# Optimization experiments

Measured on AMD Instinct MI355X. Metric: run time of the kernel, lower is better.

## Reference

```python
import jax, jax.numpy as jnp
import numpy as np


def monarch_linear(x, w1, w2, bias, out_features):
    """Monarch structured linear: permute + block-diag + permute + block-diag.
    x: (B, n_in); w1: (k, q, p); w2: (l, s, r) with k*q == l*r.
    """
    b, n = x.shape
    k, q, p = w1.shape
    l, s, r = w2.shape
    n_ext = k * p
    if n_ext > n:  # preprocess: zero-pad input to in_features_extended
        x = jnp.pad(x, ((0, 0), (0, n_ext - n)))
    # first block-diagonal matmul: (B,k,p) x (k,q,p) -> (B,k,q)
    out1 = jnp.einsum('bkp,kqp->bkq', x.reshape(b, k, p), w1)
    # permutation: view (B, k*q) as (B, r, l) then transpose -> (B, l, r)
    out1 = out1.reshape(b, r, l).transpose(0, 2, 1)
    # second block-diagonal matmul: (B,l,r) x (l,s,r) -> (B,l,s)
    out2 = jnp.einsum('blr,lsr->bls', out1, w2)
    # final permutation: (B,l,s) -> (B,s,l) -> (B, s*l), then slice to out_features
    out = out2.transpose(0, 2, 1).reshape(b, s * l)[:, :out_features]
    return out + bias


def setup_inputs() -> dict:
    key = jax.random.key(0)
    ks = jax.random.split(key, 14)
    B = 65536
    specs = {
        'x': (B, 1, 28, 28),
        'fc1_w1': (15, 27, 53), 'fc1_w2': (15, 27, 27), 'fc1_b': (392,),
        'fc2_w1': (15, 9, 27), 'fc2_w2': (15, 9, 9), 'fc2_b': (128,),
        'fc3_w1': (15, 5, 9), 'fc3_w2': (15, 5, 5), 'fc3_b': (64,),
        'fc4_w1': (15, 1, 5), 'fc4_w2': (15, 1, 1), 'fc4_b': (10,),
    }
    out = {}
    for i, (name, shape) in enumerate(specs.items()):
        v = jax.random.normal(ks[i], shape, dtype=jnp.float32)
        if name != 'x':
            v = v * 0.1  # keep activations in a sane range through 4 layers
        out[name] = v
    return out


def reference(x, fc1_w1, fc1_w2, fc1_b, fc2_w1, fc2_w2, fc2_b,
              fc3_w1, fc3_w2, fc3_b, fc4_w1, fc4_w2, fc4_b):
    gelu = lambda t: jax.nn.gelu(t, approximate=False)  # torch F.gelu default = exact erf
    h = x.reshape(x.shape[0], -1)  # flatten (B,1,28,28) -> (B,784)
    h = gelu(monarch_linear(h, fc1_w1, fc1_w2, fc1_b, 392))
    h = gelu(monarch_linear(h, fc2_w1, fc2_w2, fc2_b, 128))
    h = gelu(monarch_linear(h, fc3_w1, fc3_w2, fc3_b, 64))
    h = monarch_linear(h, fc4_w1, fc4_w2, fc4_b, 10)
    return jax.nn.log_softmax(h, axis=1)
```

## Files before the change

kernel.cpp:

```cpp
#include <hip/hip_runtime.h>
#include <hip/hip_bf16.h>

typedef unsigned short u16;
typedef unsigned int   u32;

__device__ __forceinline__ float b2f(u16 v){ return __uint_as_float(((u32)v) << 16); }
__device__ __forceinline__ u16   f2b(float f){
  u32 u = __float_as_uint(f);
  u += 0x7fffu + ((u >> 16) & 1u);
  return (u16)(u >> 16);
}
__device__ __forceinline__ float gelu_exact(float x){
  return 0.5f * x * (1.0f + erff(x * 0.70710678118654752440f));
}

__global__ __launch_bounds__(256) void k_prep_w1(
    const float* __restrict__ w1, float* __restrict__ wtg)
{
  int tid = blockIdx.x*256 + threadIdx.x;
  for (int e = tid; e < 15*54*28; e += gridDim.x*256){
    int kk = e / 1512, rem = e - kk*1512;
    int p = rem / 28, j = rem - p*28;
    wtg[e] = (p < 53 && j < 27) ? w1[(kk*27 + j)*53 + p] : 0.0f;
  }
}

__global__ __launch_bounds__(256, 5) void k_fc1a(
    const float* __restrict__ x, const float* __restrict__ wtg,
    u16* __restrict__ act, int base, int Bc)
{
  __shared__ u32 xsu[256*27];
  const int tid = threadIdx.x;
  const int k   = blockIdx.y;
  const int rowloc = blockIdx.x * 256;

  #pragma unroll 4
  for (int i = 0; i < 27; ++i){
    int e = i*256 + tid;
    int r = e / 27, c2 = e - r*27;
    int col = k*53 + 2*c2;
    const size_t rowoff = (size_t)(base + rowloc + r)*784;
    float v0 = 0.f, v1 = 0.f;
    if (col < 784) v0 = x[rowoff + col];
    if (2*c2+1 < 53 && col+1 < 784) v1 = x[rowoff + col + 1];
    xsu[e] = (u32)f2b(v0) | ((u32)f2b(v1) << 16);
  }
  __syncthreads();

  float acc[28];
  #pragma unroll
  for (int j = 0; j < 28; ++j) acc[j] = 0.0f;

  const float* __restrict__ wk = wtg + (size_t)k*1512;
  const u32* xrow = &xsu[tid*27];
  #pragma unroll
  for (int pp = 0; pp < 27; ++pp){
    const u32 xv2 = xrow[pp];
    const float x0 = __uint_as_float(xv2 << 16);
    const float x1 = __uint_as_float(xv2 & 0xffff0000u);
    const float4* wa = (const float4*)(wk + 56*pp);
    const float4* wb = (const float4*)(wk + 56*pp + 28);
    #pragma unroll
    for (int i = 0; i < 7; ++i){
      const float4 a = wa[i];
      const float4 b = wb[i];
      acc[4*i+0] = fmaf(a.x, x0, fmaf(b.x, x1, acc[4*i+0]));
      acc[4*i+1] = fmaf(a.y, x0, fmaf(b.y, x1, acc[4*i+1]));
      acc[4*i+2] = fmaf(a.z, x0, fmaf(b.z, x1, acc[4*i+2]));
      acc[4*i+3] = fmaf(a.w, x0, fmaf(b.w, x1, acc[4*i+3]));
    }
  }
  const int r0 = rowloc + tid;
  #pragma unroll
  for (int j = 0; j < 27; ++j)
    act[(size_t)(k*27 + j)*Bc + r0] = f2b(acc[j]);
}

__global__ __launch_bounds__(256) void k_fc1b(
    const float* __restrict__ w2, const float* __restrict__ b1,
    u16* act, int Bc)
{
  __shared__ __align__(16) float w2s[27*28];
  __shared__ float b1s[27];
  const int tid = threadIdx.x;
  const int l   = blockIdx.y;
  for (int e = tid; e < 27*28; e += 256){
    int s = e / 28, r = e - s*28;
    w2s[e] = (r < 27) ? w2[(l*27 + s)*27 + r] : 0.0f;
  }
  if (tid < 27){
    int m = tid*15 + l;
    b1s[tid] = (m < 392) ? b1[m] : 0.0f;
  }
  __syncthreads();

  const int row = blockIdx.x*256 + tid;
  float t[28];
  #pragma unroll
  for (int r = 0; r < 27; ++r) t[r] = b2f(act[(size_t)(r*15 + l)*Bc + row]);
  t[27] = 0.0f;
  #pragma unroll
  for (int s = 0; s < 27; ++s){
    const float* wp = &w2s[s*28];
    float va = 0.f, vb = 0.f;
    #pragma unroll
    for (int i = 0; i < 7; ++i){
      const float4 w = *(const float4*)&wp[4*i];
      va = fmaf(w.x, t[4*i+0], va); vb = fmaf(w.y, t[4*i+1], vb);
      va = fmaf(w.z, t[4*i+2], va); vb = fmaf(w.w, t[4*i+3], vb);
    }
    const int m = s*15 + l;
    float h = (m < 392) ? gelu_exact(va + vb + b1s[s]) : 0.0f;
    act[(size_t)m*Bc + row] = f2b(h);
  }
}

__global__ __launch_bounds__(256) void k_fc2a(
    const u16* __restrict__ h1t, const float* __restrict__ w1_2,
    u16* __restrict__ o2t, int Bc)
{
  __shared__ __align__(16) float ws[9*28];
  const int tid = threadIdx.x;
  const int k   = blockIdx.y;
  for (int e = tid; e < 9*28; e += 256){
    int j = e / 28, p = e - j*28;
    ws[e] = (p < 27) ? w1_2[(k*9 + j)*27 + p] : 0.0f;
  }
  __syncthreads();

  const int row = blockIdx.x*256 + tid;
  float hb[28];
  #pragma unroll
  for (int p = 0; p < 27; ++p) hb[p] = b2f(h1t[(size_t)(k*27 + p)*Bc + row]);
  hb[27] = 0.0f;
  #pragma unroll
  for (int j = 0; j < 9; ++j){
    const float* wp = &ws[j*28];
    float va = 0.f, vb = 0.f;
    #pragma unroll
    for (int i = 0; i < 7; ++i){
      const float4 w = *(const float4*)&wp[4*i];
      va = fmaf(w.x, hb[4*i+0], va); vb = fmaf(w.y, hb[4*i+1], vb);
      va = fmaf(w.z, hb[4*i+2], va); vb = fmaf(w.w, hb[4*i+3], vb);
    }
    o2t[(size_t)(k*9 + j)*Bc + row] = f2b(va + vb);
  }
}

__global__ __launch_bounds__(256) void k_fc2b(
    const u16* __restrict__ o2t, const float* __restrict__ w2_2,
    const float* __restrict__ b2, u16* __restrict__ h2t, int Bc)
{
  __shared__ float ws[9*9];
  __shared__ float b2s[9];
  const int tid = threadIdx.x;
  const int l   = blockIdx.y;
  if (tid < 81) ws[tid] = w2_2[l*81 + tid];
  if (tid < 9){
    int m = tid*15 + l;
    b2s[tid] = (m < 128) ? b2[m] : 0.0f;
  }
  __syncthreads();

  const int row = blockIdx.x*256 + tid;
  float t[9];
  #pragma unroll
  for (int r = 0; r < 9; ++r) t[r] = b2f(o2t[(size_t)(r*15 + l)*Bc + row]);
  #pragma unroll
  for (int s = 0; s < 9; ++s){
    const float* wp = &ws[s*9];
    float v = 0.f;
    #pragma unroll
    for (int r = 0; r < 9; ++r) v = fmaf(wp[r], t[r], v);
    const int m = s*15 + l;
    float h = (m < 128) ? gelu_exact(v + b2s[s]) : 0.0f;
    h2t[(size_t)m*Bc + row] = f2b(h);
  }
}

__global__ __launch_bounds__(256) void k_fc3a(
    const u16* __restrict__ h2t, const float* __restrict__ w1_3,
    u16* __restrict__ o3t, int Bc)
{
  __shared__ float ws[5*9];
  const int tid = threadIdx.x;
  const int k   = blockIdx.y;
  if (tid < 45) ws[tid] = w1_3[k*45 + tid];
  __syncthreads();

  const int row = blockIdx.x*256 + tid;
  float hb[9];
  #pragma unroll
  for (int p = 0; p < 9; ++p) hb[p] = b2f(h2t[(size_t)(k*9 + p)*Bc + row]);
  #pragma unroll
  for (int j = 0; j < 5; ++j){
    const float* wp = &ws[j*9];
    float v = 0.f;
    #pragma unroll
    for (int p = 0; p < 9; ++p) v = fmaf(wp[p], hb[p], v);
    o3t[(size_t)(k*5 + j)*Bc + row] = f2b(v);
  }
}

__global__ __launch_bounds__(256) void k_fc3b4(
    const u16* __restrict__ o3t,
    const float* __restrict__ w2_3, const float* __restrict__ b3,
    const float* __restrict__ w1_4, const float* __restrict__ w2_4, const float* __restrict__ b4,
    float* __restrict__ out, int base, int Bc)
{
  __shared__ __align__(16) float w23s[75*8];
  __shared__ float b3s[64];
  __shared__ float w14s[10*8];
  __shared__ float w24s[10];
  __shared__ float b4s[10];
  __shared__ float outS[256*10];
  const int tid = threadIdx.x;
  for (int e = tid; e < 75*8; e += 256){ int a=e/8, r=e-a*8; w23s[e] = (r<5)? w2_3[a*5+r] : 0.f; }
  for (int e = tid; e < 64;   e += 256) b3s[e] = b3[e];
  for (int e = tid; e < 80;   e += 256){ int c=e/8, p=e-c*8; w14s[e] = (p<5)? w1_4[c*5+p] : 0.f; }
  if (tid < 10){ w24s[tid] = w2_4[tid]; b4s[tid] = b4[tid]; }
  __syncthreads();

  const int rloc = blockIdx.x*256 + tid;

  float sacc[10];
  #pragma unroll
  for (int c = 0; c < 10; ++c) sacc[c] = 0.0f;

  #pragma unroll
  for (int l = 0; l < 15; ++l){
    float t[5];
    #pragma unroll
    for (int r = 0; r < 5; ++r) t[r] = b2f(o3t[(size_t)(r*15 + l)*Bc + rloc]);
    #pragma unroll
    for (int s = 0; s < 5; ++s){
      const int m = s*15 + l;
      if (m < 50){
        const float* wp = &w23s[(l*5 + s)*8];
        float v = 0.f;
        v = fmaf(wp[0], t[0], v); v = fmaf(wp[1], t[1], v);
        v = fmaf(wp[2], t[2], v); v = fmaf(wp[3], t[3], v);
        v = fmaf(wp[4], t[4], v);
        const float h = gelu_exact(v + b3s[m]);
        const int c = m / 5, p = m - (m/5)*5;
        sacc[c] = fmaf(h, w14s[c*8 + p], sacc[c]);
      }
    }
  }
  float v[10];
  #pragma unroll
  for (int c = 0; c < 10; ++c) v[c] = fmaf(sacc[c], w24s[c], b4s[c]);

  float mx = v[0];
  #pragma unroll
  for (int c = 1; c < 10; ++c) mx = fmaxf(mx, v[c]);
  float sum = 0.f;
  #pragma unroll
  for (int c = 0; c < 10; ++c) sum += expf(v[c] - mx);
  const float lse = mx + logf(sum);
  #pragma unroll
  for (int c = 0; c < 10; ++c) outS[tid*10 + c] = v[c] - lse;
  __syncthreads();
  const size_t blockOut = (size_t)(base + blockIdx.x*256) * 10;
  #pragma unroll
  for (int i = 0; i < 10; ++i){
    int e = i*256 + tid;
    out[blockOut + e] = outS[e];
  }
}

extern "C" void kernel_launch(void* const* d_in, const int* in_sizes, int n_in,
                              void* d_out, int out_size, void* d_ws, size_t ws_size,
                              hipStream_t stream)
{
  const float* x     = (const float*)d_in[0];
  const float* f1w1  = (const float*)d_in[1];
  const float* f1w2  = (const float*)d_in[2];
  const float* f1b   = (const float*)d_in[3];
  const float* f2w1  = (const float*)d_in[4];
  const float* f2w2  = (const float*)d_in[5];
  const float* f2b   = (const float*)d_in[6];
  const float* f3w1  = (const float*)d_in[7];
  const float* f3w2  = (const float*)d_in[8];
  const float* f3b   = (const float*)d_in[9];
  const float* f4w1  = (const float*)d_in[10];
  const float* f4w2  = (const float*)d_in[11];
  const float* f4b   = (const float*)d_in[12];
  const int B = in_sizes[0] / 784;
  (void)n_in; (void)out_size;

  const size_t wtgBytes = 90880;
  float* wtg = (float*)d_ws;
  u16*  wsAct = (u16*)((char*)d_ws + wtgBytes);

  k_prep_w1<<<dim3(32), 256, 0, stream>>>(f1w1, wtg);

  const size_t perRow = 750 * sizeof(u16);
  int Rc = B;
  if (ws_size - wtgBytes < (size_t)B * perRow){
    size_t rows = (ws_size - wtgBytes) / perRow;
    Rc = (int)(rows & ~(size_t)511);
    if (Rc < 512) Rc = 512;
  }
  for (int base = 0; base < B; base += Rc){
    const int Bc = (B - base < Rc) ? (B - base) : Rc;
    u16* act = wsAct;
    u16* o2t = act + (size_t)405 * Bc;
    u16* h2t = o2t + (size_t)135 * Bc;
    u16* o3t = h2t + (size_t)135 * Bc;
    k_fc1a<<<dim3(Bc/256, 15), 256, 0, stream>>>(x, wtg, act, base, Bc);
    k_fc1b<<<dim3(Bc/256, 15), 256, 0, stream>>>(f1w2, f1b, act, Bc);
    k_fc2a<<<dim3(Bc/256, 15), 256, 0, stream>>>(act, f2w1, o2t, Bc);
    k_fc2b<<<dim3(Bc/256, 15), 256, 0, stream>>>(o2t, f2w2, f2b, h2t, Bc);
    k_fc3a<<<dim3(Bc/256, 15), 256, 0, stream>>>(h2t, f3w1, o3t, Bc);
    k_fc3b4<<<dim3(Bc/256), 256, 0, stream>>>(o3t, f3w2, f3b,
                                              f4w1, f4w2, f4b, (float*)d_out, base, Bc);
  }
}
```

Before: 457.0 us.

## Compute two rows per thread in fc1/fc2a and read weights from global

The fc1a, fc1b and fc2a kernels now launch 128 threads per block, and each thread computes two batch rows. This reuses every weight load across both rows and halves the number of weight fetches per output. The fc1b and fc2a weights are pre-padded once in an extended prep kernel and read directly from global/scalar memory instead of being staged in LDS. The later kernels also drop their LDS weight staging and __syncthreads in favour of direct global reads. The trade-off is higher register pressure, roughly doubled accumulators, and fewer threads per block, which may lower occupancy.

```diff
diff --git a/kernel.cpp b/kernel.cpp
--- a/kernel.cpp
+++ b/kernel.cpp
@@ -14,18 +14,34 @@
   return 0.5f * x * (1.0f + erff(x * 0.70710678118654752440f));
 }
 
-__global__ __launch_bounds__(256) void k_prep_w1(
-    const float* __restrict__ w1, float* __restrict__ wtg)
+#define WTG_OFF   0
+#define W2G_OFF   22720
+#define W12G_OFF  34112
+#define PREP_F    37952
+
+__global__ __launch_bounds__(256) void k_prep(
+    const float* __restrict__ w1, const float* __restrict__ w2,
+    const float* __restrict__ w1_2, float* __restrict__ ws)
 {
   int tid = blockIdx.x*256 + threadIdx.x;
   for (int e = tid; e < 15*54*28; e += gridDim.x*256){
     int kk = e / 1512, rem = e - kk*1512;
     int p = rem / 28, j = rem - p*28;
-    wtg[e] = (p < 53 && j < 27) ? w1[(kk*27 + j)*53 + p] : 0.0f;
-  }
-}
-
-__global__ __launch_bounds__(256, 5) void k_fc1a(
+    ws[WTG_OFF + e] = (p < 53 && j < 27) ? w1[(kk*27 + j)*53 + p] : 0.0f;
+  }
+  for (int e = tid; e < 15*27*28; e += gridDim.x*256){
+    int l = e / 756, rem = e - l*756;
+    int s = rem / 28, r = rem - s*28;
+    ws[W2G_OFF + e] = (r < 27) ? w2[(l*27 + s)*27 + r] : 0.0f;
+  }
+  for (int e = tid; e < 15*9*28; e += gridDim.x*256){
+    int kk = e / 252, rem = e - kk*252;
+    int j = rem / 28, p = rem - j*28;
+    ws[W12G_OFF + e] = (p < 27) ? w1_2[(kk*9 + j)*27 + p] : 0.0f;
+  }
+}
+
+__global__ __launch_bounds__(128, 3) void k_fc1a(
     const float* __restrict__ x, const float* __restrict__ wtg,
     u16* __restrict__ act, int base, int Bc)
 {
@@ -35,8 +51,8 @@
   const int rowloc = blockIdx.x * 256;
 
   #pragma unroll 4
-  for (int i = 0; i < 27; ++i){
-    int e = i*256 + tid;
+  for (int i = 0; i < 54; ++i){
+    int e = i*128 + tid;
     int r = e / 27, c2 = e - r*27;
     int col = k*53 + 2*c2;
     const size_t rowoff = (size_t)(base + rowloc + r)*784;
@@ -47,103 +63,114 @@
   }
   __syncthreads();
 
-  float acc[28];
-  #pragma unroll
-  for (int j = 0; j < 28; ++j) acc[j] = 0.0f;
+  float acc0[28], acc1[28];
+  #pragma unroll
+  for (int j = 0; j < 28; ++j){ acc0[j] = 0.0f; acc1[j] = 0.0f; }
 
   const float* __restrict__ wk = wtg + (size_t)k*1512;
-  const u32* xrow = &xsu[tid*27];
+  const u32* xrow0 = &xsu[tid*27];
+  const u32* xrow1 = &xsu[(tid+128)*27];
   #pragma unroll
   for (int pp = 0; pp < 27; ++pp){
-    const u32 xv2 = xrow[pp];
-    const float x0 = __uint_as_float(xv2 << 16);
-    const float x1 = __uint_as_float(xv2 & 0xffff0000u);
+    const u32 xa = xrow0[pp];
+    const u32 xb = xrow1[pp];
+    const float x00 = __uint_as_float(xa << 16);
+    const float x01 = __uint_as_float(xa & 0xffff0000u);
+    const float x10 = __uint_as_float(xb << 16);
+    const float x11 = __uint_as_float(xb & 0xffff0000u);
     const float4* wa = (const float4*)(wk + 56*pp);
     const float4* wb = (const float4*)(wk + 56*pp + 28);
     #pragma unroll
     for (int i = 0; i < 7; ++i){
       const float4 a = wa[i];
       const float4 b = wb[i];
-      acc[4*i+0] = fmaf(a.x, x0, fmaf(b.x, x1, acc[4*i+0]));
-      acc[4*i+1] = fmaf(a.y, x0, fmaf(b.y, x1, acc[4*i+1]));
-      acc[4*i+2] = fmaf(a.z, x0, fmaf(b.z, x1, acc[4*i+2]));
-      acc[4*i+3] = fmaf(a.w, x0, fmaf(b.w, x1, acc[4*i+3]));
+      acc0[4*i+0] = fmaf(a.x, x00, fmaf(b.x, x01, acc0[4*i+0]));
+      acc0[4*i+1] = fmaf(a.y, x00, fmaf(b.y, x01, acc0[4*i+1]));
+      acc0[4*i+2] = fmaf(a.z, x00, fmaf(b.z, x01, acc0[4*i+2]));
+      acc0[4*i+3] = fmaf(a.w, x00, fmaf(b.w, x01, acc0[4*i+3]));
+      acc1[4*i+0] = fmaf(a.x, x10, fmaf(b.x, x11, acc1[4*i+0]));
+      acc1[4*i+1] = fmaf(a.y, x10, fmaf(b.y, x11, acc1[4*i+1]));
+      acc1[4*i+2] = fmaf(a.z, x10, fmaf(b.z, x11, acc1[4*i+2]));
+      acc1[4*i+3] = fmaf(a.w, x10, fmaf(b.w, x11, acc1[4*i+3]));
     }
   }
   const int r0 = rowloc + tid;
   #pragma unroll
-  for (int j = 0; j < 27; ++j)
-    act[(size_t)(k*27 + j)*Bc + r0] = f2b(acc[j]);
-}
-
-__global__ __launch_bounds__(256) void k_fc1b(
-    const float* __restrict__ w2, const float* __restrict__ b1,
+  for (int j = 0; j < 27; ++j){
+    const size_t bf = (size_t)(k*27 + j)*Bc;
+    act[bf + r0]       = f2b(acc0[j]);
+    act[bf + r0 + 128] = f2b(acc1[j]);
+  }
+}
+
+__global__ __launch_bounds__(128, 3) void k_fc1b(
+    const float* __restrict__ w2g, const float* __restrict__ b1,
     u16* act, int Bc)
 {
-  __shared__ __align__(16) float w2s[27*28];
-  __shared__ float b1s[27];
   const int tid = threadIdx.x;
   const int l   = blockIdx.y;
-  for (int e = tid; e < 27*28; e += 256){
-    int s = e / 28, r = e - s*28;
-    w2s[e] = (r < 27) ? w2[(l*27 + s)*27 + r] : 0.0f;
-  }
-  if (tid < 27){
-    int m = tid*15 + l;
-    b1s[tid] = (m < 392) ? b1[m] : 0.0f;
-  }
-  __syncthreads();
-
-  const int row = blockIdx.x*256 + tid;
-  float t[28];
-  #pragma unroll
-  for (int r = 0; r < 27; ++r) t[r] = b2f(act[(size_t)(r*15 + l)*Bc + row]);
-  t[27] = 0.0f;
+  const int row0 = blockIdx.x*256 + tid;
+  const float* __restrict__ wl = w2g + (size_t)l*756;
+
+  float t0[28], t1[28];
+  #pragma unroll
+  for (int r = 0; r < 27; ++r){
+    t0[r] = b2f(act[(size_t)(r*15 + l)*Bc + row0]);
+    t1[r] = b2f(act[(size_t)(r*15 + l)*Bc + row0 + 128]);
+  }
+  t0[27] = 0.0f; t1[27] = 0.0f;
   #pragma unroll
   for (int s = 0; s < 27; ++s){
-    const float* wp = &w2s[s*28];
-    float va = 0.f, vb = 0.f;
+    const float4* wp = (const float4*)(wl + s*28);
+    float va0=0.f, vb0=0.f, va1=0.f, vb1=0.f;
     #pragma unroll
     for (int i = 0; i < 7; ++i){
-      const float4 w = *(const float4*)&wp[4*i];
-      va = fmaf(w.x, t[4*i+0], va); vb = fmaf(w.y, t[4*i+1], vb);
-      va = fmaf(w.z, t[4*i+2], va); vb = fmaf(w.w, t[4*i+3], vb);
+      const float4 w = wp[i];
+      va0 = fmaf(w.x, t0[4*i+0], va0); vb0 = fmaf(w.y, t0[4*i+1], vb0);
+      va0 = fmaf(w.z, t0[4*i+2], va0); vb0 = fmaf(w.w, t0[4*i+3], vb0);
+      va1 = fmaf(w.x, t1[4*i+0], va1); vb1 = fmaf(w.y, t1[4*i+1], vb1);
+      va1 = fmaf(w.z, t1[4*i+2], va1); vb1 = fmaf(w.w, t1[4*i+3], vb1);
     }
     const int m = s*15 + l;
-    float h = (m < 392) ? gelu_exact(va + vb + b1s[s]) : 0.0f;
-    act[(size_t)m*Bc + row] = f2b(h);
-  }
-}
-
-__global__ __launch_bounds__(256) void k_fc2a(
-    const u16* __restrict__ h1t, const float* __restrict__ w1_2,
+    const float bb = (m < 392) ? b1[m] : 0.0f;
+    const float h0 = (m < 392) ? gelu_exact(va0 + vb0 + bb) : 0.0f;
+    const float h1 = (m < 392) ? gelu_exact(va1 + vb1 + bb) : 0.0f;
+    act[(size_t)m*Bc + row0]       = f2b(h0);
+    act[(size_t)m*Bc + row0 + 128] = f2b(h1);
+  }
+}
+
+__global__ __launch_bounds__(128, 3) void k_fc2a(
+    const u16* __restrict__ h1t, const float* __restrict__ w12g,
     u16* __restrict__ o2t, int Bc)
 {
-  __shared__ __align__(16) float ws[9*28];
   const int tid = threadIdx.x;
   const int k   = blockIdx.y;
-  for (int e = tid; e < 9*28; e += 256){
-    int j = e / 28, p = e - j*28;
-    ws[e] = (p < 27) ? w1_2[(k*9 + j)*27 + p] : 0.0f;
-  }
-  __syncthreads();
-
-  const int row = blockIdx.x*256 + tid;
-  float hb[28];
-  #pragma unroll
-  for (int p = 0; p < 27; ++p) hb[p] = b2f(h1t[(size_t)(k*27 + p)*Bc + row]);
-  hb[27] = 0.0f;
+  const int row0 = blockIdx.x*256 + tid;
+  const float* __restrict__ wk = w12g + (size_t)k*252;
+
+  float h0[28], h1[28];
+  #pragma unroll
+  for (int p = 0; p < 27; ++p){
+    h0[p] = b2f(h1t[(size_t)(k*27 + p)*Bc + row0]);
+    h1[p] = b2f(h1t[(size_t)(k*27 + p)*Bc + row0 + 128]);
+  }
+  h0[27] = 0.0f; h1[27] = 0.0f;
   #pragma unroll
   for (int j = 0; j < 9; ++j){
-    const float* wp = &ws[j*28];
-    float va = 0.f, vb = 0.f;
+    const float4* wp = (const float4*)(wk + j*28);
+    float va0=0.f, vb0=0.f, va1=0.f, vb1=0.f;
     #pragma unroll
     for (int i = 0; i < 7; ++i){
-      const float4 w = *(const float4*)&wp[4*i];
-      va = fmaf(w.x, hb[4*i+0], va); vb = fmaf(w.y, hb[4*i+1], vb);
-      va = fmaf(w.z, hb[4*i+2], va); vb = fmaf(w.w, hb[4*i+3], vb);
+      const float4 w = wp[i];
+      va0 = fmaf(w.x, h0[4*i+0], va0); vb0 = fmaf(w.y, h0[4*i+1], vb0);
+      va0 = fmaf(w.z, h0[4*i+2], va0); vb0 = fmaf(w.w, h0[4*i+3], vb0);
+      va1 = fmaf(w.x, h1[4*i+0], va1); vb1 = fmaf(w.y, h1[4*i+1], vb1);
+      va1 = fmaf(w.z, h1[4*i+2], va1); vb1 = fmaf(w.w, h1[4*i+3], vb1);
     }
-    o2t[(size_t)(k*9 + j)*Bc + row] = f2b(va + vb);
+    const size_t bf = (size_t)(k*9 + j)*Bc;
+    o2t[bf + row0]       = f2b(va0 + vb0);
+    o2t[bf + row0 + 128] = f2b(va1 + vb1);
   }
 }
 
@@ -151,16 +178,9 @@
     const u16* __restrict__ o2t, const float* __restrict__ w2_2,
     const float* __restrict__ b2, u16* __restrict__ h2t, int Bc)
 {
-  __shared__ float ws[9*9];
-  __shared__ float b2s[9];
   const int tid = threadIdx.x;
   const int l   = blockIdx.y;
-  if (tid < 81) ws[tid] = w2_2[l*81 + tid];
-  if (tid < 9){
-    int m = tid*15 + l;
-    b2s[tid] = (m < 128) ? b2[m] : 0.0f;
-  }
-  __syncthreads();
+  const float* __restrict__ wl = w2_2 + (size_t)l*81;
 
   const int row = blockIdx.x*256 + tid;
   float t[9];
@@ -168,12 +188,11 @@
   for (int r = 0; r < 9; ++r) t[r] = b2f(o2t[(size_t)(r*15 + l)*Bc + row]);
   #pragma unroll
   for (int s = 0; s < 9; ++s){
-    const float* wp = &ws[s*9];
     float v = 0.f;
     #pragma unroll
-    for (int r = 0; r < 9; ++r) v = fmaf(wp[r], t[r], v);
+    for (int r = 0; r < 9; ++r) v = fmaf(wl[s*9 + r], t[r], v);
     const int m = s*15 + l;
-    float h = (m < 128) ? gelu_exact(v + b2s[s]) : 0.0f;
+    float h = (m < 128) ? gelu_exact(v + b2[m < 128 ? m : 0]) : 0.0f;
     h2t[(size_t)m*Bc + row] = f2b(h);
   }
 }
@@ -182,11 +201,9 @@
     const u16* __restrict__ h2t, const float* __restrict__ w1_3,
     u16* __restrict__ o3t, int Bc)
 {
-  __shared__ float ws[5*9];
   const int tid = threadIdx.x;
   const int k   = blockIdx.y;
-  if (tid < 45) ws[tid] = w1_3[k*45 + tid];
-  __syncthreads();
+  const float* __restrict__ wk = w1_3 + (size_t)k*45;
 
   const int row = blockIdx.x*256 + tid;
   float hb[9];
@@ -194,10 +211,9 @@
   for (int p = 0; p < 9; ++p) hb[p] = b2f(h2t[(size_t)(k*9 + p)*Bc + row]);
   #pragma unroll
   for (int j = 0; j < 5; ++j){
-    const float* wp = &ws[j*9];
     float v = 0.f;
     #pragma unroll
-    for (int p = 0; p < 9; ++p) v = fmaf(wp[p], hb[p], v);
+    for (int p = 0; p < 9; ++p) v = fmaf(wk[j*9 + p], hb[p], v);
     o3t[(size_t)(k*5 + j)*Bc + row] = f2b(v);
   }
 }
@@ -208,19 +224,8 @@
     const float* __restrict__ w1_4, const float* __restrict__ w2_4, const float* __restrict__ b4,
     float* __restrict__ out, int base, int Bc)
 {
-  __shared__ __align__(16) float w23s[75*8];
-  __shared__ float b3s[64];
-  __shared__ float w14s[10*8];
-  __shared__ float w24s[10];
-  __shared__ float b4s[10];
   __shared__ float outS[256*10];
   const int tid = threadIdx.x;
-  for (int e = tid; e < 75*8; e += 256){ int a=e/8, r=e-a*8; w23s[e] = (r<5)? w2_3[a*5+r] : 0.f; }
-  for (int e = tid; e < 64;   e += 256) b3s[e] = b3[e];
-  for (int e = tid; e < 80;   e += 256){ int c=e/8, p=e-c*8; w14s[e] = (p<5)? w1_4[c*5+p] : 0.f; }
-  if (tid < 10){ w24s[tid] = w2_4[tid]; b4s[tid] = b4[tid]; }
-  __syncthreads();
-
   const int rloc = blockIdx.x*256 + tid;
 
   float sacc[10];
@@ -236,20 +241,20 @@
     for (int s = 0; s < 5; ++s){
       const int m = s*15 + l;
       if (m < 50){
-        const float* wp = &w23s[(l*5 + s)*8];
+        const float* wp = w2_3 + (l*5 + s)*5;
         float v = 0.f;
         v = fmaf(wp[0], t[0], v); v = fmaf(wp[1], t[1], v);
         v = fmaf(wp[2], t[2], v); v = fmaf(wp[3], t[3], v);
         v = fmaf(wp[4], t[4], v);
-        const float h = gelu_exact(v + b3s[m]);
+        const float h = gelu_exact(v + b3[m]);
         const int c = m / 5, p = m - (m/5)*5;
-        sacc[c] = fmaf(h, w14s[c*8 + p], sacc[c]);
+        sacc[c] = fmaf(h, w1_4[c*5 + p], sacc[c]);
       }
     }
   }
   float v[10];
   #pragma unroll
-  for (int c = 0; c < 10; ++c) v[c] = fmaf(sacc[c], w24s[c], b4s[c]);
+  for (int c = 0; c < 10; ++c) v[c] = fmaf(sacc[c], w2_4[c], b4[c]);
 
   float mx = v[0];
   #pragma unroll
@@ -289,16 +294,20 @@
   const int B = in_sizes[0] / 784;
   (void)n_in; (void)out_size;
 
-  const size_t wtgBytes = 90880;
-  float* wtg = (float*)d_ws;
-  u16*  wsAct = (u16*)((char*)d_ws + wtgBytes);
-
-  k_prep_w1<<<dim3(32), 256, 0, stream>>>(f1w1, wtg);
+  const size_t prepBytes = (size_t)PREP_F * sizeof(float);
+  float* wsF  = (float*)d_ws;
+  u16*  wsAct = (u16*)((char*)d_ws + prepBytes);
+
+  k_prep<<<dim3(32), 256, 0, stream>>>(f1w1, f1w2, f2w1, wsF);
+
+  const float* wtg  = wsF + WTG_OFF;
+  const float* w2g  = wsF + W2G_OFF;
+  const float* w12g = wsF + W12G_OFF;
 
   const size_t perRow = 750 * sizeof(u16);
   int Rc = B;
-  if (ws_size - wtgBytes < (size_t)B * perRow){
-    size_t rows = (ws_size - wtgBytes) / perRow;
+  if (ws_size - prepBytes < (size_t)B * perRow){
+    size_t rows = (ws_size - prepBytes) / perRow;
     Rc = (int)(rows & ~(size_t)511);
     if (Rc < 512) Rc = 512;
   }
@@ -308,9 +317,9 @@
     u16* o2t = act + (size_t)405 * Bc;
     u16* h2t = o2t + (size_t)135 * Bc;
     u16* o3t = h2t + (size_t)135 * Bc;
-    k_fc1a<<<dim3(Bc/256, 15), 256, 0, stream>>>(x, wtg, act, base, Bc);
-    k_fc1b<<<dim3(Bc/256, 15), 256, 0, stream>>>(f1w2, f1b, act, Bc);
-    k_fc2a<<<dim3(Bc/256, 15), 256, 0, stream>>>(act, f2w1, o2t, Bc);
+    k_fc1a<<<dim3(Bc/256, 15), 128, 0, stream>>>(x, wtg, act, base, Bc);
+    k_fc1b<<<dim3(Bc/256, 15), 128, 0, stream>>>(w2g, f1b, act, Bc);
+    k_fc2a<<<dim3(Bc/256, 15), 128, 0, stream>>>(act, w12g, o2t, Bc);
     k_fc2b<<<dim3(Bc/256, 15), 256, 0, stream>>>(o2t, f2w2, f2b, h2t, Bc);
     k_fc3a<<<dim3(Bc/256, 15), 256, 0, stream>>>(h2t, f3w1, o3t, Bc);
     k_fc3b4<<<dim3(Bc/256), 256, 0, stream>>>(o3t, f3w2, f3b,
```

New measurement: 601.5 us. 31.6% more time.
